# Performance work log

Hardware: AMD Instinct MI355X
Metric: run time of the kernel (lower is better)

The kernel has to match this reference:

```python
import jax, jax.numpy as jnp
import numpy as np

EPS = 1e-06

def _feature_map(x):
    # elu(x) + 1, positive feature map
    return jax.nn.elu(x) + 1.0

def setup_inputs() -> dict:
    key = jax.random.key(0)
    k1, k2, k3 = jax.random.split(key, 3)
    B, L, d_k, d_v = 2, 4096, 128, 128
    Q = jax.random.normal(k1, (B, L, d_k), dtype=jnp.float32)
    K = jax.random.normal(k2, (B, L, d_k), dtype=jnp.float32)
    V = jax.random.normal(k3, (B, L, d_v), dtype=jnp.float32)
    return {"Q": Q, "K": K, "V": V}

def reference(Q, K, V):
    # Causal linear attention (ELU feature map).
    # out_l = phi(Q_l) @ sum_{j<=l} phi(K_j)^T V_j
    # Z_l   = phi(Q_l) . sum_{j<=l} phi(K_j)
    phiQ = _feature_map(Q)                       # (B, L, dk)
    phiK = _feature_map(K)                       # (B, L, dk)
    # cumulative KV state: (B, L, dk, dv) -- parallel replacement of the
    # original per-step bmm loop
    KV = jnp.cumsum(phiK[..., :, None] * V[..., None, :], axis=1)
    out = jnp.einsum('blk,blkv->blv', phiQ, KV)  # (B, L, dv)
    Kc = jnp.cumsum(phiK, axis=1)                # (B, L, dk)
    Z = jnp.einsum('blk,blk->bl', phiQ, Kc)[..., None]  # (B, L, 1)
    return out / (Z + EPS)
```

## Files before the change

kernel.cpp:

```cpp
#include <hip/hip_runtime.h>


#define EPS 1e-6f

constexpr int Bc = 2;
constexpr int L  = 4096;
constexpr int D  = 128;
constexpr int C  = 128;
constexpr int NC = L / C;
constexpr int P  = 136;

typedef short sh8 __attribute__((ext_vector_type(8)));
typedef float f4  __attribute__((ext_vector_type(4)));

__device__ __forceinline__ float phi(float x) {
    return x > 0.0f ? x + 1.0f : __expf(x);
}
__device__ __forceinline__ unsigned short f2bf(float f) {
    unsigned u = __float_as_uint(f);
    return (unsigned short)((u + 0x7FFFu + ((u >> 16) & 1u)) >> 16);
}
__device__ __forceinline__ float bf2f(unsigned short h) {
    return __uint_as_float(((unsigned)h) << 16);
}
__device__ __forceinline__ unsigned packbf(float a, float b) {
    return (unsigned)f2bf(a) | ((unsigned)f2bf(b) << 16);
}
__device__ __forceinline__ sh8 splat1() {
    sh8 s;
#pragma unroll
    for (int j = 0; j < 8; ++j) s[j] = (short)0x3F80;
    return s;
}

__global__ __launch_bounds__(512) void k1(
    const float* __restrict__ K, const float* __restrict__ V,
    unsigned short* __restrict__ SB, float* __restrict__ Ksum) {
    const int c = blockIdx.x, b = blockIdx.y, vs = blockIdx.z;
    const int tid = threadIdx.x;
    __shared__ __align__(16) unsigned short sVT[64 * P];
    __shared__ __align__(16) unsigned short sKT[128 * P];
    const size_t base = ((size_t)b * L + (size_t)c * C) * D;

    for (int k = 0; k < 4; ++k) {
        int fi = tid + 512 * k;
        int l = fi >> 4, c4 = fi & 15;
        float4 vd = *(const float4*)(V + base + (size_t)l * D + vs * 64 + c4 * 4);
        int blk = (((l >> 3) + c4) & 15) * 8 + (l & 7);
        sVT[(c4 * 4 + 0) * P + blk] = f2bf(vd.x);
        sVT[(c4 * 4 + 1) * P + blk] = f2bf(vd.y);
        sVT[(c4 * 4 + 2) * P + blk] = f2bf(vd.z);
        sVT[(c4 * 4 + 3) * P + blk] = f2bf(vd.w);
    }
    for (int k = 0; k < 8; ++k) {
        int fi = tid + 512 * k;
        int l = fi >> 5, i4 = fi & 31;
        float4 kd = *(const float4*)(K + base + (size_t)l * D + i4 * 4);
        int blk = (((l >> 3) + i4) & 15) * 8 + (l & 7);
        sKT[(i4 * 4 + 0) * P + blk] = f2bf(phi(kd.x));
        sKT[(i4 * 4 + 1) * P + blk] = f2bf(phi(kd.y));
        sKT[(i4 * 4 + 2) * P + blk] = f2bf(phi(kd.z));
        sKT[(i4 * 4 + 3) * P + blk] = f2bf(phi(kd.w));
    }
    __syncthreads();

    const int w = tid >> 6, lane = tid & 63;
    const int r = lane & 15, q = lane >> 4;
    const int rbase = (w & 3) * 16;
    const int cbase = (w >> 2) * 64;
    const bool doK = ((w & 3) == 0);
    const sh8 ones = splat1();

    f4 acc[4], kz[4];
#pragma unroll
    for (int f = 0; f < 4; ++f) { acc[f] = {0.f,0.f,0.f,0.f}; kz[f] = {0.f,0.f,0.f,0.f}; }
#pragma unroll
    for (int ks = 0; ks < 4; ++ks) {
        int kq = ks * 4 + q;
        int vr = rbase + r;
        sh8 a = *(const sh8*)(sVT + vr * P + ((kq + (vr >> 2)) & 15) * 8);
#pragma unroll
        for (int f = 0; f < 4; ++f) {
            int ir = cbase + f * 16 + r;
            sh8 bk = *(const sh8*)(sKT + ir * P + ((kq + (ir >> 2)) & 15) * 8);
            acc[f] = __builtin_amdgcn_mfma_f32_16x16x32_bf16(a, bk, acc[f], 0, 0, 0);
            if (doK) kz[f] = __builtin_amdgcn_mfma_f32_16x16x32_bf16(ones, bk, kz[f], 0, 0, 0);
        }
    }
    unsigned short* out = SB + ((size_t)(b * NC + c)) * D * D;
#pragma unroll
    for (int f = 0; f < 4; ++f) {
        int i = cbase + f * 16 + r;
#pragma unroll
        for (int e = 0; e < 4; ++e) {
            int v = vs * 64 + rbase + q * 4 + e;
            out[(size_t)v * D + i] = f2bf(acc[f][e]);
        }
    }
    if (doK && q == 0 && vs == 0) {
#pragma unroll
        for (int f = 0; f < 4; ++f)
            Ksum[((size_t)(b * NC + c)) * D + cbase + f * 16 + r] = kz[f][0];
    }
}

__global__ __launch_bounds__(256) void k_scan(unsigned short* __restrict__ SB,
                                              float* __restrict__ Ksum) {
    const int SD = D * D;
    int idx = blockIdx.x * 256 + threadIdx.x;
    if (idx < Bc * SD) {
        int b = idx / SD, e = idx % SD;
        size_t off0 = (size_t)b * NC * SD + e;
        unsigned short vals[NC];
#pragma unroll
        for (int c = 0; c < NC; ++c) vals[c] = SB[off0 + (size_t)c * SD];
        float run = 0.0f;
#pragma unroll
        for (int c = 0; c < NC; ++c) {
            SB[off0 + (size_t)c * SD] = f2bf(run);
            run += bf2f(vals[c]);
        }
    } else if (idx < Bc * SD + Bc * D) {
        int rr = idx - Bc * SD;
        int b = rr >> 7, i = rr & 127;
        size_t off0 = (size_t)b * NC * D + i;
        float vals[NC];
#pragma unroll
        for (int c = 0; c < NC; ++c) vals[c] = Ksum[off0 + (size_t)c * D];
        float run = 0.0f;
#pragma unroll
        for (int c = 0; c < NC; ++c) {
            Ksum[off0 + (size_t)c * D] = run;
            run += vals[c];
        }
    }
}

__global__ __launch_bounds__(512) void k_out(
    const float* __restrict__ Q, const float* __restrict__ K,
    const float* __restrict__ V, const unsigned short* __restrict__ SB,
    const float* __restrict__ Ksum, float* __restrict__ Out) {
    const int c = blockIdx.x, b = blockIdx.y, rs = blockIdx.z;
    const int tid = threadIdx.x;
    __shared__ __align__(16) unsigned short sQ[32 * P];
    __shared__ __align__(16) unsigned short sK[128 * P];
    __shared__ __align__(16) unsigned short sVT[128 * P];
    __shared__ __align__(16) unsigned short sAm[32 * P];
    const size_t base  = ((size_t)b * L + (size_t)c * C) * D;
    const size_t tbase = ((size_t)(b * NC + c)) * (size_t)D * D;
    const size_t kb    = ((size_t)(b * NC + c)) * D;
    const int kceil = (rs + 1) * 32;

    uint4 sreg[4];
    {
        const uint4* sg = (const uint4*)(SB + tbase);
#pragma unroll
        for (int k = 0; k < 4; ++k) sreg[k] = sg[tid + 512 * k];
    }

    for (int k = 0; k < 2; ++k) {
        int fi = tid + 512 * k;
        int row = fi >> 5, c4 = fi & 31;
        float4 qd = *(const float4*)(Q + base + (size_t)(rs * 32 + row) * D + c4 * 4);
        uint2 pq; pq.x = packbf(phi(qd.x), phi(qd.y)); pq.y = packbf(phi(qd.z), phi(qd.w));
        *(uint2*)(sQ + row * P + c4 * 4) = pq;
    }
    for (int fi = tid; fi < kceil * 32; fi += 512) {
        int row = fi >> 5, c4 = fi & 31;
        float4 kd = *(const float4*)(K + base + (size_t)row * D + c4 * 4);
        uint2 pk; pk.x = packbf(phi(kd.x), phi(kd.y)); pk.y = packbf(phi(kd.z), phi(kd.w));
        *(uint2*)(sK + row * P + c4 * 4) = pk;
    }
    for (int fi = tid; fi < kceil * 32; fi += 512) {
        int l = fi >> 5, i4 = fi & 31;
        float4 vd = *(const float4*)(V + base + (size_t)l * D + i4 * 4);
        int blk = (((l >> 3) + i4) & 15) * 8 + (l & 7);
        sVT[(i4 * 4 + 0) * P + blk] = f2bf(vd.x);
        sVT[(i4 * 4 + 1) * P + blk] = f2bf(vd.y);
        sVT[(i4 * 4 + 2) * P + blk] = f2bf(vd.z);
        sVT[(i4 * 4 + 3) * P + blk] = f2bf(vd.w);
    }
    __syncthreads();

    const int w = tid >> 6, lane = tid & 63;
    const int r = lane & 15, q = lane >> 4;
    const int rbase = (w & 1) * 16;
    const int cq = w >> 1, cbase = cq * 32;
    const int flim = (cq <= rs) ? 2 : 0;

    sh8 bzk[4];
#pragma unroll
    for (int ks = 0; ks < 4; ++ks) {
        float4 f0 = *(const float4*)(Ksum + kb + ks * 32 + q * 8);
        float4 f1 = *(const float4*)(Ksum + kb + ks * 32 + q * 8 + 4);
        sh8 t;
        t[0] = (short)f2bf(f0.x); t[1] = (short)f2bf(f0.y);
        t[2] = (short)f2bf(f0.z); t[3] = (short)f2bf(f0.w);
        t[4] = (short)f2bf(f1.x); t[5] = (short)f2bf(f1.y);
        t[6] = (short)f2bf(f1.z); t[7] = (short)f2bf(f1.w);
        bzk[ks] = t;
    }

    f4 a2[2];
    a2[0] = {0.f,0.f,0.f,0.f}; a2[1] = {0.f,0.f,0.f,0.f};
#pragma unroll
    for (int ks = 0; ks < 4; ++ks) {
        sh8 a = *(const sh8*)(sQ + (rbase + r) * P + ks * 32 + q * 8);
        for (int f = 0; f < flim; ++f) {
            sh8 bb = *(const sh8*)(sK + (cbase + f * 16 + r) * P + ks * 32 + q * 8);
            a2[f] = __builtin_amdgcn_mfma_f32_16x16x32_bf16(a, bb, a2[f], 0, 0, 0);
        }
    }
    for (int f = 0; f < flim; ++f) {
        int j = cbase + f * 16 + r;
#pragma unroll
        for (int e = 0; e < 4; ++e) {
            int lr = rbase + q * 4 + e;
            sAm[lr * P + j] = f2bf((j <= rs * 32 + lr) ? a2[f][e] : 0.f);
        }
    }
    __syncthreads();

#pragma unroll
    for (int k = 0; k < 4; ++k) {
        int f2 = tid + 512 * k;
        *(uint4*)(sK + (f2 >> 4) * P + (f2 & 15) * 8) = sreg[k];
    }

    f4 acc[2], zacc = {0.f,0.f,0.f,0.f};
    acc[0] = {0.f,0.f,0.f,0.f}; acc[1] = {0.f,0.f,0.f,0.f};
    const sh8 ones = splat1();
    for (int ks = 0; ks <= rs; ++ks) {
        int kq = ks * 4 + q;
        sh8 am = *(const sh8*)(sAm + (rbase + r) * P + ks * 32 + q * 8);
#pragma unroll
        for (int f = 0; f < 2; ++f) {
            int vr = cbase + f * 16 + r;
            sh8 bv = *(const sh8*)(sVT + vr * P + ((kq + (vr >> 2)) & 15) * 8);
            acc[f] = __builtin_amdgcn_mfma_f32_16x16x32_bf16(am, bv, acc[f], 0, 0, 0);
        }
        zacc = __builtin_amdgcn_mfma_f32_16x16x32_bf16(am, ones, zacc, 0, 0, 0);
    }
    __syncthreads();

#pragma unroll
    for (int ks = 0; ks < 4; ++ks) {
        sh8 a = *(const sh8*)(sQ + (rbase + r) * P + ks * 32 + q * 8);
#pragma unroll
        for (int f = 0; f < 2; ++f) {
            sh8 bs = *(const sh8*)(sK + (cbase + f * 16 + r) * P + ks * 32 + q * 8);
            acc[f] = __builtin_amdgcn_mfma_f32_16x16x32_bf16(a, bs, acc[f], 0, 0, 0);
        }
        zacc = __builtin_amdgcn_mfma_f32_16x16x32_bf16(a, bzk[ks], zacc, 0, 0, 0);
    }

#pragma unroll
    for (int e = 0; e < 4; ++e) {
        int lr = rbase + q * 4 + e;
        float rz = 1.0f / (zacc[e] + EPS);
#pragma unroll
        for (int f = 0; f < 2; ++f) {
            int v = cbase + f * 16 + r;
            Out[base + (size_t)(rs * 32 + lr) * D + v] = acc[f][e] * rz;
        }
    }
}

extern "C" void kernel_launch(void* const* d_in, const int* in_sizes, int n_in,
                              void* d_out, int out_size, void* d_ws, size_t ws_size,
                              hipStream_t stream) {
    const float* Q = (const float*)d_in[0];
    const float* K = (const float*)d_in[1];
    const float* V = (const float*)d_in[2];
    float* Out = (float*)d_out;
    unsigned short* SBw = (unsigned short*)d_ws;
    float* Ksum = (float*)((char*)d_ws + (size_t)Bc * NC * D * D * 2);

    k1<<<dim3(NC, Bc, 2), 512, 0, stream>>>(K, V, SBw, Ksum);
    int total = Bc * D * D + Bc * D;
    k_scan<<<dim3((total + 255) / 256), 256, 0, stream>>>(SBw, Ksum);
    k_out<<<dim3(NC, Bc, 4), 512, 0, stream>>>(Q, K, V, SBw, Ksum, Out);
}
```

Before: 92.11 us.

## Load MFMA operands for Q, K and state directly from global into registers

The output kernel no longer stages phi(Q), phi(K) and the chunk state matrix in shared memory. Each lane loads its MFMA fragments straight from global memory and applies phi plus the bf16 conversion in registers, which drops two LDS arrays and a barrier and lowers LDS use, possibly raising occupancy. The causal-skip logic is removed: every block now loads all of V and computes the full QK^T tile, relying on the mask, instead of bounding work by rs. This adds redundant global reads and compute for the early row slices, and the uncoalesced per-lane row loads may cost bandwidth.

```diff
diff --git a/kernel.cpp b/kernel.cpp
--- a/kernel.cpp
+++ b/kernel.cpp
@@ -31,6 +31,16 @@
 #pragma unroll
     for (int j = 0; j < 8; ++j) s[j] = (short)0x3F80;
     return s;
+}
+__device__ __forceinline__ sh8 ldphi8(const float* p) {
+    float4 f0 = *(const float4*)(p);
+    float4 f1 = *(const float4*)(p + 4);
+    sh8 t;
+    t[0] = (short)f2bf(phi(f0.x)); t[1] = (short)f2bf(phi(f0.y));
+    t[2] = (short)f2bf(phi(f0.z)); t[3] = (short)f2bf(phi(f0.w));
+    t[4] = (short)f2bf(phi(f1.x)); t[5] = (short)f2bf(phi(f1.y));
+    t[6] = (short)f2bf(phi(f1.z)); t[7] = (short)f2bf(phi(f1.w));
+    return t;
 }
 
 __global__ __launch_bounds__(512) void k1(
@@ -142,36 +152,27 @@
     const float* __restrict__ Ksum, float* __restrict__ Out) {
     const int c = blockIdx.x, b = blockIdx.y, rs = blockIdx.z;
     const int tid = threadIdx.x;
-    __shared__ __align__(16) unsigned short sQ[32 * P];
-    __shared__ __align__(16) unsigned short sK[128 * P];
     __shared__ __align__(16) unsigned short sVT[128 * P];
     __shared__ __align__(16) unsigned short sAm[32 * P];
     const size_t base  = ((size_t)b * L + (size_t)c * C) * D;
     const size_t tbase = ((size_t)(b * NC + c)) * (size_t)D * D;
     const size_t kb    = ((size_t)(b * NC + c)) * D;
-    const int kceil = (rs + 1) * 32;
-
-    uint4 sreg[4];
+
+    const int w = tid >> 6, lane = tid & 63;
+    const int r = lane & 15, q = lane >> 4;
+    const int rbase = (w & 1) * 16;
+    const int cq = w >> 1, cbase = cq * 32;
+
+    sh8 aq[4];
     {
-        const uint4* sg = (const uint4*)(SB + tbase);
-#pragma unroll
-        for (int k = 0; k < 4; ++k) sreg[k] = sg[tid + 512 * k];
-    }
-
-    for (int k = 0; k < 2; ++k) {
+        const float* qrow = Q + base + (size_t)(rs * 32 + rbase + r) * D;
+#pragma unroll
+        for (int ks = 0; ks < 4; ++ks) aq[ks] = ldphi8(qrow + ks * 32 + q * 8);
+    }
+
+#pragma unroll
+    for (int k = 0; k < 8; ++k) {
         int fi = tid + 512 * k;
-        int row = fi >> 5, c4 = fi & 31;
-        float4 qd = *(const float4*)(Q + base + (size_t)(rs * 32 + row) * D + c4 * 4);
-        uint2 pq; pq.x = packbf(phi(qd.x), phi(qd.y)); pq.y = packbf(phi(qd.z), phi(qd.w));
-        *(uint2*)(sQ + row * P + c4 * 4) = pq;
-    }
-    for (int fi = tid; fi < kceil * 32; fi += 512) {
-        int row = fi >> 5, c4 = fi & 31;
-        float4 kd = *(const float4*)(K + base + (size_t)row * D + c4 * 4);
-        uint2 pk; pk.x = packbf(phi(kd.x), phi(kd.y)); pk.y = packbf(phi(kd.z), phi(kd.w));
-        *(uint2*)(sK + row * P + c4 * 4) = pk;
-    }
-    for (int fi = tid; fi < kceil * 32; fi += 512) {
         int l = fi >> 5, i4 = fi & 31;
         float4 vd = *(const float4*)(V + base + (size_t)l * D + i4 * 4);
         int blk = (((l >> 3) + i4) & 15) * 8 + (l & 7);
@@ -180,38 +181,22 @@
         sVT[(i4 * 4 + 2) * P + blk] = f2bf(vd.z);
         sVT[(i4 * 4 + 3) * P + blk] = f2bf(vd.w);
     }
-    __syncthreads();
-
-    const int w = tid >> 6, lane = tid & 63;
-    const int r = lane & 15, q = lane >> 4;
-    const int rbase = (w & 1) * 16;
-    const int cq = w >> 1, cbase = cq * 32;
-    const int flim = (cq <= rs) ? 2 : 0;
-
-    sh8 bzk[4];
-#pragma unroll
-    for (int ks = 0; ks < 4; ++ks) {
-        float4 f0 = *(const float4*)(Ksum + kb + ks * 32 + q * 8);
-        float4 f1 = *(const float4*)(Ksum + kb + ks * 32 + q * 8 + 4);
-        sh8 t;
-        t[0] = (short)f2bf(f0.x); t[1] = (short)f2bf(f0.y);
-        t[2] = (short)f2bf(f0.z); t[3] = (short)f2bf(f0.w);
-        t[4] = (short)f2bf(f1.x); t[5] = (short)f2bf(f1.y);
-        t[6] = (short)f2bf(f1.z); t[7] = (short)f2bf(f1.w);
-        bzk[ks] = t;
-    }
 
     f4 a2[2];
     a2[0] = {0.f,0.f,0.f,0.f}; a2[1] = {0.f,0.f,0.f,0.f};
-#pragma unroll
-    for (int ks = 0; ks < 4; ++ks) {
-        sh8 a = *(const sh8*)(sQ + (rbase + r) * P + ks * 32 + q * 8);
-        for (int f = 0; f < flim; ++f) {
-            sh8 bb = *(const sh8*)(sK + (cbase + f * 16 + r) * P + ks * 32 + q * 8);
-            a2[f] = __builtin_amdgcn_mfma_f32_16x16x32_bf16(a, bb, a2[f], 0, 0, 0);
-        }
-    }
-    for (int f = 0; f < flim; ++f) {
+    {
+        const float* krow0 = K + base + (size_t)(cbase + r) * D;
+        const float* krow1 = K + base + (size_t)(cbase + 16 + r) * D;
+#pragma unroll
+        for (int ks = 0; ks < 4; ++ks) {
+            sh8 b0 = ldphi8(krow0 + ks * 32 + q * 8);
+            sh8 b1 = ldphi8(krow1 + ks * 32 + q * 8);
+            a2[0] = __builtin_amdgcn_mfma_f32_16x16x32_bf16(aq[ks], b0, a2[0], 0, 0, 0);
+            a2[1] = __builtin_amdgcn_mfma_f32_16x16x32_bf16(aq[ks], b1, a2[1], 0, 0, 0);
+        }
+    }
+#pragma unroll
+    for (int f = 0; f < 2; ++f) {
         int j = cbase + f * 16 + r;
 #pragma unroll
         for (int e = 0; e < 4; ++e) {
@@ -221,16 +206,11 @@
     }
     __syncthreads();
 
-#pragma unroll
-    for (int k = 0; k < 4; ++k) {
-        int f2 = tid + 512 * k;
-        *(uint4*)(sK + (f2 >> 4) * P + (f2 & 15) * 8) = sreg[k];
-    }
-
     f4 acc[2], zacc = {0.f,0.f,0.f,0.f};
     acc[0] = {0.f,0.f,0.f,0.f}; acc[1] = {0.f,0.f,0.f,0.f};
     const sh8 ones = splat1();
-    for (int ks = 0; ks <= rs; ++ks) {
+#pragma unroll
+    for (int ks = 0; ks < 4; ++ks) {
         int kq = ks * 4 + q;
         sh8 am = *(const sh8*)(sAm + (rbase + r) * P + ks * 32 + q * 8);
 #pragma unroll
@@ -241,17 +221,25 @@
         }
         zacc = __builtin_amdgcn_mfma_f32_16x16x32_bf16(am, ones, zacc, 0, 0, 0);
     }
-    __syncthreads();
-
-#pragma unroll
-    for (int ks = 0; ks < 4; ++ks) {
-        sh8 a = *(const sh8*)(sQ + (rbase + r) * P + ks * 32 + q * 8);
-#pragma unroll
-        for (int f = 0; f < 2; ++f) {
-            sh8 bs = *(const sh8*)(sK + (cbase + f * 16 + r) * P + ks * 32 + q * 8);
-            acc[f] = __builtin_amdgcn_mfma_f32_16x16x32_bf16(a, bs, acc[f], 0, 0, 0);
-        }
-        zacc = __builtin_amdgcn_mfma_f32_16x16x32_bf16(a, bzk[ks], zacc, 0, 0, 0);
+
+    {
+        const unsigned short* srow0 = SB + tbase + (size_t)(cbase + r) * D;
+        const unsigned short* srow1 = SB + tbase + (size_t)(cbase + 16 + r) * D;
+#pragma unroll
+        for (int ks = 0; ks < 4; ++ks) {
+            sh8 bs0 = *(const sh8*)(srow0 + ks * 32 + q * 8);
+            sh8 bs1 = *(const sh8*)(srow1 + ks * 32 + q * 8);
+            float4 f0 = *(const float4*)(Ksum + kb + ks * 32 + q * 8);
+            float4 f1 = *(const float4*)(Ksum + kb + ks * 32 + q * 8 + 4);
+            sh8 bz;
+            bz[0] = (short)f2bf(f0.x); bz[1] = (short)f2bf(f0.y);
+            bz[2] = (short)f2bf(f0.z); bz[3] = (short)f2bf(f0.w);
+            bz[4] = (short)f2bf(f1.x); bz[5] = (short)f2bf(f1.y);
+            bz[6] = (short)f2bf(f1.z); bz[7] = (short)f2bf(f1.w);
+            acc[0] = __builtin_amdgcn_mfma_f32_16x16x32_bf16(aq[ks], bs0, acc[0], 0, 0, 0);
+            acc[1] = __builtin_amdgcn_mfma_f32_16x16x32_bf16(aq[ks], bs1, acc[1], 0, 0, 0);
+            zacc   = __builtin_amdgcn_mfma_f32_16x16x32_bf16(aq[ks], bz, zacc, 0, 0, 0);
+        }
     }
 
 #pragma unroll
```

New measurement: 81.65 us. 11.4% less time.
